# Performance work log

Hardware: AMD Instinct MI355X
Metric: run time of the kernel (lower is better)

The kernel has to match this reference:

```python
import jax, jax.numpy as jnp
import numpy as np

B, D, H, E, K = 16384, 1024, 4096, 8, 2   # batch, d_model, expert hidden, experts, top_k
GH = 256                                    # gating hidden (hard-coded in GatingNetwork)


def setup_inputs() -> dict:
    key = jax.random.key(0)
    ks = jax.random.split(key, 6)
    sd = 0.02
    return {
        "x":   jax.random.normal(ks[0], (B, D), jnp.float32),
        # gating network params
        "gw1": jax.random.normal(ks[1], (D, GH), jnp.float32) * sd,
        "gb1": jnp.zeros((GH,), jnp.float32),
        "gw2": jax.random.normal(ks[2], (GH, E), jnp.float32) * sd,
        "gb2": jnp.zeros((E,), jnp.float32),
        # stacked expert MLP params: Linear(D,H) -> tanh -> Linear(H,D)
        "ew1": jax.random.normal(ks[3], (E, D, H), jnp.float32) * sd,
        "eb1": jnp.zeros((E, H), jnp.float32),
        "ew2": jax.random.normal(ks[4], (E, H, D), jnp.float32) * sd,
        "eb2": jnp.zeros((E, D), jnp.float32),
    }


def reference(x, gw1, gb1, gw2, gb2, ew1, eb1, ew2, eb2):
    # Gating: Linear -> ReLU -> (dropout=eval identity) -> Linear
    router_logits = jax.nn.relu(x @ gw1 + gb1) @ gw2 + gb2          # [B, E]
    router_probs = jax.nn.softmax(router_logits, axis=-1)
    topk_probs, topk_idx = jax.lax.top_k(router_probs, K)           # [B, K]
    topk_probs = topk_probs / topk_probs.sum(axis=-1, keepdims=True)
    # Dense combine weights [B, E]: normalized top-k prob for selected experts, 0 else.
    combine = jnp.sum(
        jax.nn.one_hot(topk_idx, E, dtype=x.dtype) * topk_probs[:, :, None], axis=1
    )                                                               # [B, E]
    # Equivalent to per-token top-k dispatch: non-selected experts have weight 0.
    out = jnp.zeros_like(x)
    for e in range(E):  # small fixed expert count
        ye = jnp.tanh(x @ ew1[e] + eb1[e]) @ ew2[e] + eb2[e]        # [B, D]
        out = out + combine[:, e:e + 1] * ye
    return out, topk_idx
```

## Files before the change

kernel.cpp:

```cpp
#include <hip/hip_runtime.h>
#include <stdint.h>

#define B_TOK 16384
#define D_MODEL 1024
#define H_EXP 4096
#define N_EXP 8
#define SLOT_MAX 33792

typedef unsigned int u32;
typedef unsigned short u16;
typedef __attribute__((ext_vector_type(8))) short short8;
typedef __attribute__((ext_vector_type(4))) float f32x4;

__device__ __forceinline__ u16 f2bf(float f) {
  u32 u = __float_as_uint(f);
  u32 r = (u + 0x7fffu + ((u >> 16) & 1u)) >> 16;
  return (u16)r;
}

__device__ __forceinline__ void gl_lds16(const void* g, void* l) {
  __builtin_amdgcn_global_load_lds(
      (const __attribute__((address_space(1))) u32*)g,
      (__attribute__((address_space(3))) u32*)l, 16, 0, 0);
}

__global__ __launch_bounds__(256) void k_gate_h(
    const float* __restrict__ x, const float* __restrict__ gw1,
    const float* __restrict__ gb1, float* __restrict__ hbuf)
{
  __shared__ float As[16][132];
  __shared__ float Bs[16][128];
  int m0 = blockIdx.x * 128, n0 = blockIdx.y * 128;
  int tid = threadIdx.x;
  int tx = tid & 15, ty = tid >> 4;
  float acc[8][8] = {};
  for (int kt = 0; kt < 1024; kt += 16) {
#pragma unroll
    for (int i = 0; i < 8; ++i) {
      int idx = tid + 256 * i;
      int r = idx >> 4, c = idx & 15;
      As[c][r] = x[(size_t)(m0 + r) * 1024 + kt + c];
    }
#pragma unroll
    for (int i = 0; i < 8; ++i) {
      int idx = tid + 256 * i;
      int r = idx >> 7, c = idx & 127;
      Bs[r][c] = gw1[(size_t)(kt + r) * 256 + n0 + c];
    }
    __syncthreads();
#pragma unroll
    for (int k = 0; k < 16; ++k) {
      float a[8], b[8];
#pragma unroll
      for (int mi = 0; mi < 8; ++mi) a[mi] = As[k][ty * 8 + mi];
#pragma unroll
      for (int ni = 0; ni < 8; ++ni) b[ni] = Bs[k][tx * 8 + ni];
#pragma unroll
      for (int mi = 0; mi < 8; ++mi)
#pragma unroll
        for (int ni = 0; ni < 8; ++ni)
          acc[mi][ni] += a[mi] * b[ni];
    }
    __syncthreads();
  }
#pragma unroll
  for (int mi = 0; mi < 8; ++mi) {
    int m = m0 + ty * 8 + mi;
#pragma unroll
    for (int ni = 0; ni < 8; ++ni) {
      int n = n0 + tx * 8 + ni;
      float v = acc[mi][ni] + gb1[n];
      hbuf[(size_t)m * 256 + n] = v > 0.f ? v : 0.f;
    }
  }
}

__global__ __launch_bounds__(256) void k_gate_top2(
    const float* __restrict__ hbuf, const float* __restrict__ gw2,
    const float* __restrict__ gb2, int* __restrict__ tok_idx,
    float* __restrict__ tok_w, float* __restrict__ out_idx)
{
  int wave = threadIdx.x >> 6, lane = threadIdx.x & 63;
  int t = blockIdx.x * 4 + wave;
  float v[8] = {};
  const float* hr = hbuf + (size_t)t * 256;
#pragma unroll
  for (int i = 0; i < 4; ++i) {
    int j = lane + 64 * i;
    float h = hr[j];
#pragma unroll
    for (int e = 0; e < 8; ++e) v[e] += h * gw2[j * 8 + e];
  }
#pragma unroll
  for (int off = 32; off; off >>= 1) {
#pragma unroll
    for (int e = 0; e < 8; ++e) v[e] += __shfl_down(v[e], off);
  }
  if (lane == 0) {
    float l[8];
#pragma unroll
    for (int e = 0; e < 8; ++e) l[e] = v[e] + gb2[e];
    int i1 = 0; float b1 = l[0];
#pragma unroll
    for (int e = 1; e < 8; ++e) { if (l[e] > b1) { b1 = l[e]; i1 = e; } }
    int i2 = -1; float b2 = -3.4e38f;
#pragma unroll
    for (int e = 0; e < 8; ++e) { if (e == i1) continue; if (l[e] > b2) { b2 = l[e]; i2 = e; } }
    float w1 = 1.f / (1.f + expf(b2 - b1));
    float w2 = 1.f - w1;
    tok_idx[t * 2] = i1; tok_idx[t * 2 + 1] = i2;
    tok_w[t * 2] = w1;  tok_w[t * 2 + 1] = w2;
    out_idx[t * 2] = (float)i1; out_idx[t * 2 + 1] = (float)i2;
  }
}

__global__ __launch_bounds__(256) void k_count(const int* __restrict__ tok_idx,
                                               int* __restrict__ counts)
{
  __shared__ int h[8];
  if (threadIdx.x < 8) h[threadIdx.x] = 0;
  __syncthreads();
  int4 v = ((const int4*)tok_idx)[blockIdx.x * 256 + threadIdx.x];
  atomicAdd(&h[v.x], 1); atomicAdd(&h[v.y], 1);
  atomicAdd(&h[v.z], 1); atomicAdd(&h[v.w], 1);
  __syncthreads();
  if (threadIdx.x < 8) atomicAdd(&counts[threadIdx.x], h[threadIdx.x]);
}

__global__ void k_offsets(const int* counts, int* offs) {
  if (threadIdx.x == 0) {
    int acc = 0;
    for (int e = 0; e < 8; ++e) { offs[e] = acc; acc += (counts[e] + 127) & ~127; }
    offs[8] = acc;
  }
}

__global__ __launch_bounds__(256) void k_perm_init(int* perm, float* aw) {
  int i = blockIdx.x * 256 + threadIdx.x;
  if (i < SLOT_MAX) { perm[i] = 0; aw[i] = 0.f; }
}

__global__ __launch_bounds__(256) void k_scatter(
    const int* __restrict__ tok_idx, const float* __restrict__ tok_w,
    const int* __restrict__ offs, int* __restrict__ counts2,
    int* __restrict__ perm, float* __restrict__ aw)
{
  __shared__ int lcnt[8], lbase[8];
  int tid = threadIdx.x;
  if (tid < 8) lcnt[tid] = 0;
  __syncthreads();
  int t = blockIdx.x * 256 + tid;
  int e0 = tok_idx[t * 2], e1 = tok_idx[t * 2 + 1];
  int r0 = atomicAdd(&lcnt[e0], 1);
  int r1 = atomicAdd(&lcnt[e1], 1);
  __syncthreads();
  if (tid < 8) lbase[tid] = atomicAdd(&counts2[tid], lcnt[tid]);
  __syncthreads();
  int s0 = offs[e0] + lbase[e0] + r0;
  int s1 = offs[e1] + lbase[e1] + r1;
  perm[s0] = t; aw[s0] = tok_w[t * 2];
  perm[s1] = t; aw[s1] = tok_w[t * 2 + 1];
}

__global__ __launch_bounds__(256) void k_cast_x(const float* __restrict__ x,
                                                u16* __restrict__ xb) {
  int i = (blockIdx.x * 256 + threadIdx.x) * 4;
  const float4 v = *(const float4*)(x + i);
  ushort4 o;
  o.x = f2bf(v.x); o.y = f2bf(v.y); o.z = f2bf(v.z); o.w = f2bf(v.w);
  *(ushort4*)(xb + i) = o;
}

__global__ __launch_bounds__(256) void k_trans(
    const float* __restrict__ in, u16* __restrict__ out,
    int in_stride, int row_off, int col_off, int out_stride,
    int in_esz, int out_esz)
{
  __shared__ float tile[32][33];
  int e = blockIdx.z;
  in += (size_t)e * in_esz;
  out += (size_t)e * out_esz;
  int n0 = blockIdx.x * 32, m0 = blockIdx.y * 32;
  int tx = threadIdx.x & 31, ty = threadIdx.x >> 5;
#pragma unroll
  for (int i = 0; i < 4; ++i)
    tile[ty + i * 8][tx] =
        in[(size_t)(row_off + m0 + ty + i * 8) * in_stride + col_off + n0 + tx];
  __syncthreads();
#pragma unroll
  for (int i = 0; i < 4; ++i)
    out[(size_t)(n0 + ty + i * 8) * out_stride + m0 + tx] = f2bf(tile[tx][ty + i * 8]);
}

__device__ __forceinline__ int find_expert(const int* offs, int m0) {
  int e = 0;
#pragma unroll
  for (int i = 1; i < 8; ++i) e += (m0 >= offs[i]);
  return e;
}

__global__ __launch_bounds__(256) void k_gemm1(
    const u16* __restrict__ xb, const u16* __restrict__ wTc,
    const float* __restrict__ eb1, const int* __restrict__ offs,
    const int* __restrict__ perm, u16* __restrict__ y1,
    int h0, int Hc)
{
  int m0 = blockIdx.x * 128;
  if (m0 >= offs[8]) return;
  int e = find_expert(offs, m0);
  int hcol0 = blockIdx.y * 128;

  __shared__ u16 As[128 * 32];
  __shared__ u16 Bs[128 * 32];

  int tid = threadIdx.x, lane = tid & 63, wave = tid >> 6;
  int kq = lane & 3;
  const u16* wbase = wTc + (size_t)e * Hc * 1024;
  const u16* aptr[2]; const u16* bptr[2]; u16* alds[2]; u16* blds[2];
#pragma unroll
  for (int it = 0; it < 2; ++it) {
    int chunk = wave * 2 + it;
    int r = chunk * 16 + (lane >> 2);
    int tok = perm[m0 + r];
    aptr[it] = xb + (size_t)tok * 1024 + kq * 8;
    bptr[it] = wbase + (size_t)(hcol0 + r) * 1024 + kq * 8;
    alds[it] = As + chunk * 512 + lane * 8;
    blds[it] = Bs + chunk * 512 + lane * 8;
  }

  f32x4 acc[4][4] = {};
  int wm = (wave & 1) * 64, wn = (wave >> 1) * 64;
  int frow = lane & 15, fq = lane >> 4;

  for (int kt = 0; kt < 1024; kt += 32) {
#pragma unroll
    for (int it = 0; it < 2; ++it) {
      gl_lds16(aptr[it] + kt, alds[it]);
      gl_lds16(bptr[it] + kt, blds[it]);
    }
    __syncthreads();
    short8 af[4], bf[4];
#pragma unroll
    for (int i = 0; i < 4; ++i)
      af[i] = *(const short8*)(As + (wm + i * 16 + frow) * 32 + fq * 8);
#pragma unroll
    for (int j = 0; j < 4; ++j)
      bf[j] = *(const short8*)(Bs + (wn + j * 16 + frow) * 32 + fq * 8);
#pragma unroll
    for (int i = 0; i < 4; ++i)
#pragma unroll
      for (int j = 0; j < 4; ++j)
        acc[i][j] = __builtin_amdgcn_mfma_f32_16x16x32_bf16(af[i], bf[j], acc[i][j], 0, 0, 0);
    __syncthreads();
  }

  int col = lane & 15, qr = (lane >> 4) * 4;
#pragma unroll
  for (int j = 0; j < 4; ++j) {
    int n = wn + j * 16 + col;
    float bias = eb1[e * 4096 + h0 + hcol0 + n];
#pragma unroll
    for (int i = 0; i < 4; ++i) {
#pragma unroll
      for (int r = 0; r < 4; ++r) {
        int m = wm + i * 16 + qr + r;
        float v = tanhf(acc[i][j][r] + bias);
        y1[(size_t)(m0 + m) * Hc + hcol0 + n] = f2bf(v);
      }
    }
  }
}

__global__ __launch_bounds__(256) void k_gemm2(
    const u16* __restrict__ y1, const u16* __restrict__ wTc,
    const float* __restrict__ eb2, const int* __restrict__ offs,
    const int* __restrict__ perm, const float* __restrict__ aw,
    float* __restrict__ out, int h0, int Hc)
{
  int m0 = blockIdx.x * 128;
  if (m0 >= offs[8]) return;
  int e = find_expert(offs, m0);
  int n0 = blockIdx.y * 128;

  __shared__ u16 As[128 * 32];
  __shared__ u16 Bs[128 * 32];

  int tid = threadIdx.x, lane = tid & 63, wave = tid >> 6;
  int kq = lane & 3;
  const u16* wbase = wTc + (size_t)e * 1024 * Hc;
  const u16* aptr[2]; const u16* bptr[2]; u16* alds[2]; u16* blds[2];
#pragma unroll
  for (int it = 0; it < 2; ++it) {
    int chunk = wave * 2 + it;
    int r = chunk * 16 + (lane >> 2);
    aptr[it] = y1 + (size_t)(m0 + r) * Hc + kq * 8;
    bptr[it] = wbase + (size_t)(n0 + r) * Hc + kq * 8;
    alds[it] = As + chunk * 512 + lane * 8;
    blds[it] = Bs + chunk * 512 + lane * 8;
  }

  f32x4 acc[4][4] = {};
  int wm = (wave & 1) * 64, wn = (wave >> 1) * 64;
  int frow = lane & 15, fq = lane >> 4;

  for (int kt = 0; kt < Hc; kt += 32) {
#pragma unroll
    for (int it = 0; it < 2; ++it) {
      gl_lds16(aptr[it] + kt, alds[it]);
      gl_lds16(bptr[it] + kt, blds[it]);
    }
    __syncthreads();
    short8 af[4], bf[4];
#pragma unroll
    for (int i = 0; i < 4; ++i)
      af[i] = *(const short8*)(As + (wm + i * 16 + frow) * 32 + fq * 8);
#pragma unroll
    for (int j = 0; j < 4; ++j)
      bf[j] = *(const short8*)(Bs + (wn + j * 16 + frow) * 32 + fq * 8);
#pragma unroll
    for (int i = 0; i < 4; ++i)
#pragma unroll
      for (int j = 0; j < 4; ++j)
        acc[i][j] = __builtin_amdgcn_mfma_f32_16x16x32_bf16(af[i], bf[j], acc[i][j], 0, 0, 0);
    __syncthreads();
  }

  int col = lane & 15, qr = (lane >> 4) * 4;
#pragma unroll
  for (int i = 0; i < 4; ++i) {
    int tokv[4]; float wv[4];
#pragma unroll
    for (int r = 0; r < 4; ++r) {
      int slot = m0 + wm + i * 16 + qr + r;
      tokv[r] = perm[slot];
      wv[r] = aw[slot];
    }
#pragma unroll
    for (int j = 0; j < 4; ++j) {
      int d = n0 + wn + j * 16 + col;
      float bias = (h0 == 0) ? eb2[e * 1024 + d] : 0.f;
#pragma unroll
      for (int r = 0; r < 4; ++r) {
        float v = acc[i][j][r] + bias;
        atomicAdd(out + (size_t)tokv[r] * 1024 + d, wv[r] * v);
      }
    }
  }
}

extern "C" void kernel_launch(void* const* d_in, const int* in_sizes, int n_in,
                              void* d_out, int out_size, void* d_ws, size_t ws_size,
                              hipStream_t stream)
{
  const float* x   = (const float*)d_in[0];
  const float* gw1 = (const float*)d_in[1];
  const float* gb1 = (const float*)d_in[2];
  const float* gw2 = (const float*)d_in[3];
  const float* gb2 = (const float*)d_in[4];
  const float* ew1 = (const float*)d_in[5];
  const float* eb1 = (const float*)d_in[6];
  const float* ew2 = (const float*)d_in[7];
  const float* eb2 = (const float*)d_in[8];
  float* out = (float*)d_out;

  char* ws = (char*)d_ws;
  int*   counts  = (int*)(ws + 0);
  int*   counts2 = (int*)(ws + 32);
  int*   offs    = (int*)(ws + 64);
  int*   tok_idx = (int*)(ws + 256);
  float* tok_w   = (float*)(ws + 131328);
  int*   perm    = (int*)(ws + 262400);
  float* aw      = (float*)(ws + 397568);
  u16*   xb      = (u16*)(ws + 1048576);
  char*  wbase   = ws + 34603008;

  int Hc = 256;
  for (int c = 4096; c >= 256; c >>= 1) {
    if (34603008ull + 83968ull * c <= ws_size) { Hc = c; break; }
  }
  u16*   wTc  = (u16*)wbase;
  u16*   y1   = (u16*)(wbase + (size_t)16384 * Hc);
  float* hbuf = (float*)y1;

  hipMemsetAsync(d_out, 0, (size_t)B_TOK * D_MODEL * 4, stream);
  hipMemsetAsync(d_ws, 0, 64, stream);

  k_gate_h<<<dim3(128, 2), 256, 0, stream>>>(x, gw1, gb1, hbuf);
  k_gate_top2<<<4096, 256, 0, stream>>>(hbuf, gw2, gb2, tok_idx, tok_w,
                                        out + (size_t)B_TOK * D_MODEL);
  k_count<<<32, 256, 0, stream>>>(tok_idx, counts);
  k_offsets<<<1, 64, 0, stream>>>(counts, offs);
  k_perm_init<<<132, 256, 0, stream>>>(perm, aw);
  k_scatter<<<64, 256, 0, stream>>>(tok_idx, tok_w, offs, counts2, perm, aw);
  k_cast_x<<<16384, 256, 0, stream>>>(x, xb);

  for (int h0 = 0; h0 < 4096; h0 += Hc) {
    k_trans<<<dim3(Hc / 32, 32, 8), 256, 0, stream>>>(
        ew1, wTc, 4096, 0, h0, 1024, 1024 * 4096, Hc * 1024);
    k_gemm1<<<dim3(SLOT_MAX / 128, Hc / 128), 256, 0, stream>>>(
        xb, wTc, eb1, offs, perm, y1, h0, Hc);
    k_trans<<<dim3(32, Hc / 32, 8), 256, 0, stream>>>(
        ew2, wTc, 1024, h0, 0, Hc, 4096 * 1024, 1024 * Hc);
    k_gemm2<<<dim3(SLOT_MAX / 128, 8), 256, 0, stream>>>(
        y1, wTc, eb2, offs, perm, aw, out, h0, Hc);
  }
}
```

Measured before the change: 1.682 ms.

## Swizzle LDS tiles, swap grid axes, and use fast tanh in expert GEMMs

```diff
diff --git a/kernel.cpp b/kernel.cpp
--- a/kernel.cpp
+++ b/kernel.cpp
@@ -16,6 +16,12 @@
   u32 u = __float_as_uint(f);
   u32 r = (u + 0x7fffu + ((u >> 16) & 1u)) >> 16;
   return (u16)r;
+}
+
+__device__ __forceinline__ float fast_tanh(float x) {
+  x = fminf(15.f, fmaxf(-15.f, x));
+  float t = __expf(2.f * x);
+  return (t - 1.f) / (t + 1.f);
 }
 
 __device__ __forceinline__ void gl_lds16(const void* g, void* l) {
@@ -205,16 +211,17 @@
     const int* __restrict__ perm, u16* __restrict__ y1,
     int h0, int Hc)
 {
-  int m0 = blockIdx.x * 128;
+  int m0 = blockIdx.y * 128;
   if (m0 >= offs[8]) return;
   int e = find_expert(offs, m0);
-  int hcol0 = blockIdx.y * 128;
+  int hcol0 = blockIdx.x * 128;
 
   __shared__ u16 As[128 * 32];
   __shared__ u16 Bs[128 * 32];
 
   int tid = threadIdx.x, lane = tid & 63, wave = tid >> 6;
   int kq = lane & 3;
+  int ks = kq ^ ((lane >> 3) & 3);
   const u16* wbase = wTc + (size_t)e * Hc * 1024;
   const u16* aptr[2]; const u16* bptr[2]; u16* alds[2]; u16* blds[2];
 #pragma unroll
@@ -222,8 +229,8 @@
     int chunk = wave * 2 + it;
     int r = chunk * 16 + (lane >> 2);
     int tok = perm[m0 + r];
-    aptr[it] = xb + (size_t)tok * 1024 + kq * 8;
-    bptr[it] = wbase + (size_t)(hcol0 + r) * 1024 + kq * 8;
+    aptr[it] = xb + (size_t)tok * 1024 + ks * 8;
+    bptr[it] = wbase + (size_t)(hcol0 + r) * 1024 + ks * 8;
     alds[it] = As + chunk * 512 + lane * 8;
     blds[it] = Bs + chunk * 512 + lane * 8;
   }
@@ -231,6 +238,7 @@
   f32x4 acc[4][4] = {};
   int wm = (wave & 1) * 64, wn = (wave >> 1) * 64;
   int frow = lane & 15, fq = lane >> 4;
+  int fqs = fq ^ ((frow >> 1) & 3);
 
   for (int kt = 0; kt < 1024; kt += 32) {
 #pragma unroll
@@ -242,10 +250,10 @@
     short8 af[4], bf[4];
 #pragma unroll
     for (int i = 0; i < 4; ++i)
-      af[i] = *(const short8*)(As + (wm + i * 16 + frow) * 32 + fq * 8);
+      af[i] = *(const short8*)(As + (wm + i * 16 + frow) * 32 + fqs * 8);
 #pragma unroll
     for (int j = 0; j < 4; ++j)
-      bf[j] = *(const short8*)(Bs + (wn + j * 16 + frow) * 32 + fq * 8);
+      bf[j] = *(const short8*)(Bs + (wn + j * 16 + frow) * 32 + fqs * 8);
 #pragma unroll
     for (int i = 0; i < 4; ++i)
 #pragma unroll
@@ -264,7 +272,7 @@
 #pragma unroll
       for (int r = 0; r < 4; ++r) {
         int m = wm + i * 16 + qr + r;
-        float v = tanhf(acc[i][j][r] + bias);
+        float v = fast_tanh(acc[i][j][r] + bias);
         y1[(size_t)(m0 + m) * Hc + hcol0 + n] = f2bf(v);
       }
     }
@@ -277,24 +285,25 @@
     const int* __restrict__ perm, const float* __restrict__ aw,
     float* __restrict__ out, int h0, int Hc)
 {
-  int m0 = blockIdx.x * 128;
+  int m0 = blockIdx.y * 128;
   if (m0 >= offs[8]) return;
   int e = find_expert(offs, m0);
-  int n0 = blockIdx.y * 128;
+  int n0 = blockIdx.x * 128;
 
   __shared__ u16 As[128 * 32];
   __shared__ u16 Bs[128 * 32];
 
   int tid = threadIdx.x, lane = tid & 63, wave = tid >> 6;
   int kq = lane & 3;
+  int ks = kq ^ ((lane >> 3) & 3);
   const u16* wbase = wTc + (size_t)e * 1024 * Hc;
   const u16* aptr[2]; const u16* bptr[2]; u16* alds[2]; u16* blds[2];
 #pragma unroll
   for (int it = 0; it < 2; ++it) {
     int chunk = wave * 2 + it;
     int r = chunk * 16 + (lane >> 2);
-    aptr[it] = y1 + (size_t)(m0 + r) * Hc + kq * 8;
-    bptr[it] = wbase + (size_t)(n0 + r) * Hc + kq * 8;
+    aptr[it] = y1 + (size_t)(m0 + r) * Hc + ks * 8;
+    bptr[it] = wbase + (size_t)(n0 + r) * Hc + ks * 8;
     alds[it] = As + chunk * 512 + lane * 8;
     blds[it] = Bs + chunk * 512 + lane * 8;
   }
@@ -302,6 +311,7 @@
   f32x4 acc[4][4] = {};
   int wm = (wave & 1) * 64, wn = (wave >> 1) * 64;
   int frow = lane & 15, fq = lane >> 4;
+  int fqs = fq ^ ((frow >> 1) & 3);
 
   for (int kt = 0; kt < Hc; kt += 32) {
 #pragma unroll
@@ -313,10 +323,10 @@
     short8 af[4], bf[4];
 #pragma unroll
     for (int i = 0; i < 4; ++i)
-      af[i] = *(const short8*)(As + (wm + i * 16 + frow) * 32 + fq * 8);
+      af[i] = *(const short8*)(As + (wm + i * 16 + frow) * 32 + fqs * 8);
 #pragma unroll
     for (int j = 0; j < 4; ++j)
-      bf[j] = *(const short8*)(Bs + (wn + j * 16 + frow) * 32 + fq * 8);
+      bf[j] = *(const short8*)(Bs + (wn + j * 16 + frow) * 32 + fqs * 8);
 #pragma unroll
     for (int i = 0; i < 4; ++i)
 #pragma unroll
@@ -397,11 +407,11 @@
   for (int h0 = 0; h0 < 4096; h0 += Hc) {
     k_trans<<<dim3(Hc / 32, 32, 8), 256, 0, stream>>>(
         ew1, wTc, 4096, 0, h0, 1024, 1024 * 4096, Hc * 1024);
-    k_gemm1<<<dim3(SLOT_MAX / 128, Hc / 128), 256, 0, stream>>>(
+    k_gemm1<<<dim3(Hc / 128, SLOT_MAX / 128), 256, 0, stream>>>(
         xb, wTc, eb1, offs, perm, y1, h0, Hc);
     k_trans<<<dim3(32, Hc / 32, 8), 256, 0, stream>>>(
         ew2, wTc, 1024, h0, 0, Hc, 4096 * 1024, 1024 * Hc);
-    k_gemm2<<<dim3(SLOT_MAX / 128, 8), 256, 0, stream>>>(
+    k_gemm2<<<dim3(8, SLOT_MAX / 128), 256, 0, stream>>>(
         y1, wTc, eb2, offs, perm, aw, out, h0, Hc);
   }
 }
```

New measurement: 1.428 ms. -15.1%, faster.
